# Performance work log

Measured on AMD Instinct MI355X. Metric: run time of the kernel, lower is better.

## Reference

```python
import jax, jax.numpy as jnp
import numpy as np

H = 8  # number of heads


def setup_inputs() -> dict:
    key = jax.random.key(0)
    ks = jax.random.split(key, 5)
    B, L, D = 4, 2048, 512
    scale = 1.0 / np.sqrt(D)
    return {
        "query": jax.random.normal(ks[0], (B, L, D), dtype=jnp.float32),
        "keys": jax.random.normal(ks[1], (B, L, D), dtype=jnp.float32),
        "Wq": jax.random.normal(ks[2], (D, D), dtype=jnp.float32) * scale,
        "Wk": jax.random.normal(ks[3], (D, D), dtype=jnp.float32) * scale,
        "Wv": jax.random.normal(ks[4], (D, D), dtype=jnp.float32) * scale,
    }


def reference(query, keys, Wq, Wk, Wv):
    B, Lq, D = query.shape
    Lk = keys.shape[1]
    dh = D // H
    # Linear layers (torch nn.Linear: y = x @ W.T), then split heads.
    Q = (query @ Wq.T).reshape(B, Lq, H, dh)
    K = (keys @ Wk.T).reshape(B, Lk, H, dh)
    V = (keys @ Wv.T).reshape(B, Lk, H, dh)
    # NOTE: original scales by sqrt(key_dim) == sqrt(D), not sqrt(head_dim).
    inv_scale = 1.0 / jnp.sqrt(jnp.float32(D))
    scores = jnp.einsum("bqhd,bkhd->bhqk", Q, K) * inv_scale  # [B,H,Lq,Lk]
    attn = jax.nn.softmax(scores, axis=-1)
    # dropout_p = 0 (eval); no dropout applied.
    out = jnp.einsum("bhqk,bkhd->bqhd", attn, V).reshape(B, Lq, D)
    return out + query  # residual
```

## Files before the change

### kernel.cpp

```cpp
#include <hip/hip_runtime.h>

typedef unsigned short u16;
typedef unsigned int   u32;
typedef short  s16x8  __attribute__((ext_vector_type(8)));
typedef float  f32x16 __attribute__((ext_vector_type(16)));
typedef unsigned int u32x2 __attribute__((ext_vector_type(2)));

__device__ __forceinline__ u16 f2bf(float f) {
    union { u32 i; float f; } x; x.f = f;
    return (u16)((x.i + 0x8000u) >> 16);
}
__device__ __forceinline__ u32 cvt_pk_bf16(float a, float b) {
    u32 r;
    asm("v_cvt_pk_bf16_f32 %0, %1, %2" : "=v"(r) : "v"(a), "v"(b));
    return r;
}
__device__ __forceinline__ u32x2 pl32_swap2(u32 vdst, u32 vsrc) {
#if __has_builtin(__builtin_amdgcn_permlane32_swap)
    return __builtin_amdgcn_permlane32_swap(vdst, vsrc, false, false);
#else
    asm("v_permlane32_swap_b32 %0, %1" : "+v"(vdst), "+v"(vsrc));
    u32x2 r; r.x = vdst; r.y = vsrc; return r;
#endif
}

#define PD 512

__global__ __launch_bounds__(256) void proj_mfma(
    const float* __restrict__ query, const float* __restrict__ keys,
    const float* __restrict__ Wq, const float* __restrict__ Wk, const float* __restrict__ Wv,
    u16* __restrict__ Qo, u16* __restrict__ Ko, u16* __restrict__ Vt)
{
    const int z = blockIdx.z;
    const float* __restrict__ X = (z == 0) ? query : keys;
    const float* __restrict__ W = (z == 0) ? Wq : ((z == 1) ? Wk : Wv);
    const int bx = blockIdx.x;
    const int by = blockIdx.y;

    const float* __restrict__ Amat = (z < 2) ? X : W;
    const float* __restrict__ Bmat = (z < 2) ? W : X;
    const int a0 = ((z < 2) ? bx : by) * 128;
    const int b0 = ((z < 2) ? by : bx) * 128;

    __shared__ u16 As[128][40];
    __shared__ u16 Bs[128][40];

    const int tid  = threadIdx.x;
    const int wave = tid >> 6, lane = tid & 63;
    const int wm = wave >> 1, wn = wave & 1;
    const int l31 = lane & 31, lh = lane >> 5;

    const int srow = tid >> 1;
    const int sk   = (tid & 1) * 16;

    f32x16 acc[2][2];
    #pragma unroll
    for (int i = 0; i < 2; ++i)
        #pragma unroll
        for (int j = 0; j < 2; ++j)
            #pragma unroll
            for (int r = 0; r < 16; ++r) acc[i][j][r] = 0.f;

    float4 ra[4], rb[4];
    {
        const float* ap = Amat + (size_t)(a0 + srow) * PD + sk;
        const float* bp = Bmat + (size_t)(b0 + srow) * PD + sk;
        #pragma unroll
        for (int i = 0; i < 4; ++i) {
            ra[i] = *(const float4*)(ap + 4*i);
            rb[i] = *(const float4*)(bp + 4*i);
        }
    }

    for (int k0 = 0; k0 < PD; k0 += 32) {
        __syncthreads();
        {
            u32 aw[8], bw[8];
            #pragma unroll
            for (int i = 0; i < 4; ++i) {
                aw[2*i]   = cvt_pk_bf16(ra[i].x, ra[i].y);
                aw[2*i+1] = cvt_pk_bf16(ra[i].z, ra[i].w);
                bw[2*i]   = cvt_pk_bf16(rb[i].x, rb[i].y);
                bw[2*i+1] = cvt_pk_bf16(rb[i].z, rb[i].w);
            }
            *(uint4*)&As[srow][sk]     = *(uint4*)&aw[0];
            *(uint4*)&As[srow][sk + 8] = *(uint4*)&aw[4];
            *(uint4*)&Bs[srow][sk]     = *(uint4*)&bw[0];
            *(uint4*)&Bs[srow][sk + 8] = *(uint4*)&bw[4];
        }
        if (k0 + 32 < PD) {
            const float* ap = Amat + (size_t)(a0 + srow) * PD + (k0 + 32) + sk;
            const float* bp = Bmat + (size_t)(b0 + srow) * PD + (k0 + 32) + sk;
            #pragma unroll
            for (int i = 0; i < 4; ++i) {
                ra[i] = *(const float4*)(ap + 4*i);
                rb[i] = *(const float4*)(bp + 4*i);
            }
        }
        __syncthreads();

        #pragma unroll
        for (int ks = 0; ks < 2; ++ks) {
            s16x8 af[2], bfr[2];
            #pragma unroll
            for (int mf = 0; mf < 2; ++mf) {
                uint4 v = *(uint4*)&As[wm*64 + mf*32 + l31][ks*16 + lh*8];
                af[mf] = *(s16x8*)&v;
            }
            #pragma unroll
            for (int nf = 0; nf < 2; ++nf) {
                uint4 v = *(uint4*)&Bs[wn*64 + nf*32 + l31][ks*16 + lh*8];
                bfr[nf] = *(s16x8*)&v;
            }
            #pragma unroll
            for (int mf = 0; mf < 2; ++mf)
                #pragma unroll
                for (int nf = 0; nf < 2; ++nf)
                    acc[mf][nf] = __builtin_amdgcn_mfma_f32_32x32x16_bf16(
                        af[mf], bfr[nf], acc[mf][nf], 0, 0, 0);
        }
    }

    const float osc = (z == 0) ? (0.044194173824159216f * 1.4426950408889634f) : 1.0f;
    u16* __restrict__ O = (z == 0) ? Qo : Ko;
    #pragma unroll
    for (int mf = 0; mf < 2; ++mf)
        #pragma unroll
        for (int nf = 0; nf < 2; ++nf)
            #pragma unroll
            for (int r = 0; r < 16; ++r) {
                const int mi = a0 + wm*64 + mf*32 + (r & 3) + 8*(r >> 2) + 4*lh;
                const int ni = b0 + wn*64 + nf*32 + l31;
                const u16 v = f2bf(acc[mf][nf][r] * osc);
                if (z < 2) {
                    O[(size_t)mi * PD + ni] = v;
                } else {
                    const int bb_ = ni >> 11, ll = ni & 2047;
                    Vt[((size_t)(bb_ * 512 + mi)) * 2048 + ll] = v;
                }
            }
}

__global__ __launch_bounds__(512) void attn_mfma(
    const u16* __restrict__ Qp, const u16* __restrict__ Kp, const u16* __restrict__ Vt,
    const float* __restrict__ query, float* __restrict__ out)
{
    const int qt = blockIdx.x;
    const int h  = blockIdx.y;
    const int b  = blockIdx.z;
    const int q0 = qt * 128;
    const int L = 2048;

    __shared__ uint4 lds_u4[73728 / 16];
    u16* lds16 = (u16*)lds_u4;

    const int tid  = threadIdx.x;
    const int wave = tid >> 6;
    const int grp  = wave >> 2;
    const int sw   = wave & 3;
    const int lane = tid & 63;
    const int l31 = lane & 31, lh = lane >> 5;

    u16* gb16 = lds16 + grp * 18432;
    u16* KsA  = gb16;
    u16* VtsA = gb16 + 4608;
    u16* KsB  = gb16 + 9216;
    u16* VtsB = gb16 + 13824;

    const int qrow = b * L + q0 + sw * 32 + l31;
    s16x8 qf[4];
    #pragma unroll
    for (int ds = 0; ds < 4; ++ds) {
        uint4 v = *(const uint4*)(Qp + (size_t)qrow * PD + h*64 + ds*16 + lh*8);
        qf[ds] = *(s16x8*)&v;
    }

    f32x16 ot[2];
    #pragma unroll
    for (int mf = 0; mf < 2; ++mf)
        #pragma unroll
        for (int r = 0; r < 16; ++r) ot[mf][r] = 0.f;
    float l_i = 0.f;

    const int gtid = tid & 255;
    const int srow = gtid >> 2;
    const int sc   = (gtid & 3) * 16;

    const u16* kpB = Kp + (size_t)(b*L + grp*64 + srow) * PD + h*64 + sc;
    const u16* vpB = Vt + ((size_t)((b*8 + h)*64 + srow)) * 2048 + grp*64 + sc;

    uint4 rkA0, rkA1, rvA0, rvA1, rkB0, rkB1, rvB0, rvB1;

#define A_LOADG(k0v, rk0, rk1, rv0, rv1) { \
    const u16* kp_ = kpB + (size_t)(k0v) * PD; \
    const u16* vp_ = vpB + (k0v); \
    rk0 = *(const uint4*)kp_;      rk1 = *(const uint4*)(kp_ + 8); \
    rv0 = *(const uint4*)vp_;      rv1 = *(const uint4*)(vp_ + 8); }

#define A_STOREL(Ks, Vts, rk0, rk1, rv0, rv1) { \
    *(uint4*)&(Ks)[srow*72 + sc]      = rk0; \
    *(uint4*)&(Ks)[srow*72 + sc + 8]  = rk1; \
    *(uint4*)&(Vts)[srow*72 + sc]     = rv0; \
    *(uint4*)&(Vts)[srow*72 + sc + 8] = rv1; }

    auto compute = [&](const u16* Ks, const u16* Vts) {
        f32x16 s[2];
        #pragma unroll
        for (int kf = 0; kf < 2; ++kf) {
            #pragma unroll
            for (int r = 0; r < 16; ++r) s[kf][r] = 0.f;
            #pragma unroll
            for (int ds = 0; ds < 4; ++ds) {
                uint4 av = *(uint4*)&Ks[(kf*32 + l31)*72 + ds*16 + lh*8];
                s[kf] = __builtin_amdgcn_mfma_f32_32x32x16_bf16(
                    *(s16x8*)&av, qf[ds], s[kf], 0, 0, 0);
            }
        }
        float rs = 0.f;
        u32 pq[2][4][2];
        #pragma unroll
        for (int kf = 0; kf < 2; ++kf)
            #pragma unroll
            for (int g = 0; g < 4; ++g) {
                float p0 = __builtin_amdgcn_exp2f(s[kf][4*g+0]);
                float p1 = __builtin_amdgcn_exp2f(s[kf][4*g+1]);
                float p2 = __builtin_amdgcn_exp2f(s[kf][4*g+2]);
                float p3 = __builtin_amdgcn_exp2f(s[kf][4*g+3]);
                rs += (p0 + p1) + (p2 + p3);
                pq[kf][g][0] = cvt_pk_bf16(p0, p1);
                pq[kf][g][1] = cvt_pk_bf16(p2, p3);
            }
        rs += __shfl_xor(rs, 32);
        l_i += rs;
        #pragma unroll
        for (int s4 = 0; s4 < 4; ++s4) {
            const int kf = s4 >> 1, ga = (s4 & 1) * 2;
            u32x2 r0 = pl32_swap2(pq[kf][ga][0], pq[kf][ga+1][0]);
            u32x2 r1 = pl32_swap2(pq[kf][ga][1], pq[kf][ga+1][1]);
            union { u32 w[4]; s16x8 v; } bu;
            bu.w[0] = r0.x; bu.w[1] = r1.x; bu.w[2] = r0.y; bu.w[3] = r1.y;
            #pragma unroll
            for (int mf = 0; mf < 2; ++mf) {
                uint4 av = *(uint4*)&Vts[(mf*32 + l31)*72 + s4*16 + lh*8];
                ot[mf] = __builtin_amdgcn_mfma_f32_32x32x16_bf16(
                    *(s16x8*)&av, bu.v, ot[mf], 0, 0, 0);
            }
        }
    };

    A_LOADG(0, rkA0, rkA1, rvA0, rvA1);
    A_STOREL(KsA, VtsA, rkA0, rkA1, rvA0, rvA1);
    A_LOADG(128, rkB0, rkB1, rvB0, rvB1);
    __syncthreads();

    #pragma unroll 1
    for (int j = 0; j < 16; j += 2) {
        {
            const int kn = (j + 2 < 16) ? (j + 2) * 128 : j * 128;
            A_LOADG(kn, rkA0, rkA1, rvA0, rvA1);
        }
        A_STOREL(KsB, VtsB, rkB0, rkB1, rvB0, rvB1);
        __builtin_amdgcn_s_setprio(1);
        compute(KsA, VtsA);
        __builtin_amdgcn_s_setprio(0);
        __syncthreads();
        {
            const int kn = (j + 3 < 16) ? (j + 3) * 128 : (j + 1) * 128;
            A_LOADG(kn, rkB0, rkB1, rvB0, rvB1);
        }
        A_STOREL(KsA, VtsA, rkA0, rkA1, rvA0, rvA1);
        __builtin_amdgcn_s_setprio(1);
        compute(KsB, VtsB);
        __builtin_amdgcn_s_setprio(0);
        __syncthreads();
    }

    float* Ppart = (float*)lds_u4;
    float* l_p   = Ppart + 128*68;
    float* Oe    = (float*)lds_u4 + 36864/4;

    if (grp == 1) {
        #pragma unroll
        for (int mf = 0; mf < 2; ++mf)
            #pragma unroll
            for (int g = 0; g < 4; ++g) {
                float4 v;
                v.x = ot[mf][g*4+0]; v.y = ot[mf][g*4+1];
                v.z = ot[mf][g*4+2]; v.w = ot[mf][g*4+3];
                const int dh0 = mf*32 + 8*g + 4*lh;
                *(float4*)&Ppart[(sw*32 + l31)*68 + dh0] = v;
            }
        if (lh == 0) l_p[sw*32 + l31] = l_i;
    }
    __syncthreads();
    if (grp == 0) {
        const float inv_l = 1.0f / (l_i + l_p[sw*32 + l31]);
        #pragma unroll
        for (int mf = 0; mf < 2; ++mf)
            #pragma unroll
            for (int g = 0; g < 4; ++g) {
                const int dh0 = mf*32 + 8*g + 4*lh;
                float4 pv = *(float4*)&Ppart[(sw*32 + l31)*68 + dh0];
                float4 v;
                v.x = (ot[mf][g*4+0] + pv.x) * inv_l;
                v.y = (ot[mf][g*4+1] + pv.y) * inv_l;
                v.z = (ot[mf][g*4+2] + pv.z) * inv_l;
                v.w = (ot[mf][g*4+3] + pv.w) * inv_l;
                *(float4*)&Oe[(sw*32 + l31)*68 + dh0] = v;
            }
    }
    __syncthreads();
    {
        const int r  = tid >> 2;
        const int c0 = (tid & 3) * 16;
        const size_t gb = ((size_t)(b*L + q0 + r)) * PD + h*64 + c0;
        #pragma unroll
        for (int i = 0; i < 4; ++i) {
            float4 ov = *(float4*)&Oe[r*68 + c0 + 4*i];
            float4 qv = *(const float4*)(query + gb + 4*i);
            ov.x += qv.x; ov.y += qv.y; ov.z += qv.z; ov.w += qv.w;
            *(float4*)(out + gb + 4*i) = ov;
        }
    }
}

extern "C" void kernel_launch(void* const* d_in, const int* in_sizes, int n_in,
                              void* d_out, int out_size, void* d_ws, size_t ws_size,
                              hipStream_t stream) {
    const float* query = (const float*)d_in[0];
    const float* keys  = (const float*)d_in[1];
    const float* Wq    = (const float*)d_in[2];
    const float* Wk    = (const float*)d_in[3];
    const float* Wv    = (const float*)d_in[4];
    float* out = (float*)d_out;

    u16* Qp = (u16*)d_ws;
    u16* Kp = Qp + (size_t)8192 * 512;
    u16* Vt = Kp + (size_t)8192 * 512;

    proj_mfma<<<dim3(64, 4, 3), 256, 0, stream>>>(query, keys, Wq, Wk, Wv, Qp, Kp, Vt);
    attn_mfma<<<dim3(16, 8, 4), 512, 0, stream>>>(Qp, Kp, Vt, query, out);
}
```

Before: 166.6 us.

## Single-buffer K/V in LDS to halve shared memory and remap block order

Measured after the change: 160.2 us. -3.8%, faster.

```diff
diff --git a/kernel.cpp b/kernel.cpp
--- a/kernel.cpp
+++ b/kernel.cpp
@@ -145,13 +145,15 @@
     const u16* __restrict__ Qp, const u16* __restrict__ Kp, const u16* __restrict__ Vt,
     const float* __restrict__ query, float* __restrict__ out)
 {
-    const int qt = blockIdx.x;
-    const int h  = blockIdx.y;
-    const int b  = blockIdx.z;
+    const int flat = blockIdx.x + 16 * blockIdx.y + 128 * blockIdx.z;
+    const int src  = (flat & 7) * 64 + (flat >> 3);
+    const int qt = src & 15;
+    const int h  = (src >> 4) & 7;
+    const int b  = src >> 7;
     const int q0 = qt * 128;
     const int L = 2048;
 
-    __shared__ uint4 lds_u4[73728 / 16];
+    __shared__ uint4 lds_u4[36864 / 16];
     u16* lds16 = (u16*)lds_u4;
 
     const int tid  = threadIdx.x;
@@ -161,11 +163,9 @@
     const int lane = tid & 63;
     const int l31 = lane & 31, lh = lane >> 5;
 
-    u16* gb16 = lds16 + grp * 18432;
-    u16* KsA  = gb16;
-    u16* VtsA = gb16 + 4608;
-    u16* KsB  = gb16 + 9216;
-    u16* VtsB = gb16 + 13824;
+    u16* gb16 = lds16 + grp * 9216;
+    u16* Ks   = gb16;
+    u16* Vts  = gb16 + 4608;
 
     const int qrow = b * L + q0 + sw * 32 + l31;
     s16x8 qf[4];
@@ -189,21 +189,21 @@
     const u16* kpB = Kp + (size_t)(b*L + grp*64 + srow) * PD + h*64 + sc;
     const u16* vpB = Vt + ((size_t)((b*8 + h)*64 + srow)) * 2048 + grp*64 + sc;
 
-    uint4 rkA0, rkA1, rvA0, rvA1, rkB0, rkB1, rvB0, rvB1;
-
-#define A_LOADG(k0v, rk0, rk1, rv0, rv1) { \
+    uint4 rk0, rk1, rv0, rv1;
+
+#define A_LOADG(k0v) { \
     const u16* kp_ = kpB + (size_t)(k0v) * PD; \
     const u16* vp_ = vpB + (k0v); \
     rk0 = *(const uint4*)kp_;      rk1 = *(const uint4*)(kp_ + 8); \
     rv0 = *(const uint4*)vp_;      rv1 = *(const uint4*)(vp_ + 8); }
 
-#define A_STOREL(Ks, Vts, rk0, rk1, rv0, rv1) { \
-    *(uint4*)&(Ks)[srow*72 + sc]      = rk0; \
-    *(uint4*)&(Ks)[srow*72 + sc + 8]  = rk1; \
-    *(uint4*)&(Vts)[srow*72 + sc]     = rv0; \
-    *(uint4*)&(Vts)[srow*72 + sc + 8] = rv1; }
-
-    auto compute = [&](const u16* Ks, const u16* Vts) {
+#define A_STOREL() { \
+    *(uint4*)&Ks [srow*72 + sc]      = rk0; \
+    *(uint4*)&Ks [srow*72 + sc + 8]  = rk1; \
+    *(uint4*)&Vts[srow*72 + sc]      = rv0; \
+    *(uint4*)&Vts[srow*72 + sc + 8]  = rv1; }
+
+    auto compute = [&]() {
         f32x16 s[2];
         #pragma unroll
         for (int kf = 0; kf < 2; ++kf) {
@@ -248,37 +248,23 @@
         }
     };
 
-    A_LOADG(0, rkA0, rkA1, rvA0, rvA1);
-    A_STOREL(KsA, VtsA, rkA0, rkA1, rvA0, rvA1);
-    A_LOADG(128, rkB0, rkB1, rvB0, rvB1);
-    __syncthreads();
-
+    A_LOADG(0);
     #pragma unroll 1
-    for (int j = 0; j < 16; j += 2) {
-        {
-            const int kn = (j + 2 < 16) ? (j + 2) * 128 : j * 128;
-            A_LOADG(kn, rkA0, rkA1, rvA0, rvA1);
-        }
-        A_STOREL(KsB, VtsB, rkB0, rkB1, rvB0, rvB1);
+    for (int j = 0; j < 16; ++j) {
+        __syncthreads();
+        A_STOREL();
+        if (j + 1 < 16) A_LOADG((j + 1) * 128);
+        __syncthreads();
         __builtin_amdgcn_s_setprio(1);
-        compute(KsA, VtsA);
+        compute();
         __builtin_amdgcn_s_setprio(0);
-        __syncthreads();
-        {
-            const int kn = (j + 3 < 16) ? (j + 3) * 128 : (j + 1) * 128;
-            A_LOADG(kn, rkB0, rkB1, rvB0, rvB1);
-        }
-        A_STOREL(KsA, VtsA, rkA0, rkA1, rvA0, rvA1);
-        __builtin_amdgcn_s_setprio(1);
-        compute(KsB, VtsB);
-        __builtin_amdgcn_s_setprio(0);
-        __syncthreads();
     }
 
     float* Ppart = (float*)lds_u4;
     float* l_p   = Ppart + 128*68;
-    float* Oe    = (float*)lds_u4 + 36864/4;
-
+    float* Oe    = (float*)lds_u4;
+
+    __syncthreads();
     if (grp == 1) {
         #pragma unroll
         for (int mf = 0; mf < 2; ++mf)
@@ -301,11 +287,22 @@
             for (int g = 0; g < 4; ++g) {
                 const int dh0 = mf*32 + 8*g + 4*lh;
                 float4 pv = *(float4*)&Ppart[(sw*32 + l31)*68 + dh0];
+                ot[mf][g*4+0] = (ot[mf][g*4+0] + pv.x) * inv_l;
+                ot[mf][g*4+1] = (ot[mf][g*4+1] + pv.y) * inv_l;
+                ot[mf][g*4+2] = (ot[mf][g*4+2] + pv.z) * inv_l;
+                ot[mf][g*4+3] = (ot[mf][g*4+3] + pv.w) * inv_l;
+            }
+    }
+    __syncthreads();
+    if (grp == 0) {
+        #pragma unroll
+        for (int mf = 0; mf < 2; ++mf)
+            #pragma unroll
+            for (int g = 0; g < 4; ++g) {
                 float4 v;
-                v.x = (ot[mf][g*4+0] + pv.x) * inv_l;
-                v.y = (ot[mf][g*4+1] + pv.y) * inv_l;
-                v.z = (ot[mf][g*4+2] + pv.z) * inv_l;
-                v.w = (ot[mf][g*4+3] + pv.w) * inv_l;
+                v.x = ot[mf][g*4+0]; v.y = ot[mf][g*4+1];
+                v.z = ot[mf][g*4+2]; v.w = ot[mf][g*4+3];
+                const int dh0 = mf*32 + 8*g + 4*lh;
                 *(float4*)&Oe[(sw*32 + l31)*68 + dh0] = v;
             }
     }
```
